# Kernel optimization log

Measured on AMD Instinct MI355X. Metric: run time of the kernel, lower is better.

Reference implementation:

```python
import jax, jax.numpy as jnp
import numpy as np

# Fixed directional 3x3 stencils (order j=0..3 as in the torch module)
_K0 = [[0, 0, 0], [-0.5, 1, -0.5], [0, 0, 0]]
_K1 = [[0, 0, -0.5], [0, 1, 0], [-0.5, 0, 0]]
_K2 = [[0, -0.5, 0], [0, 1, 0], [0, -0.5, 0]]
_K3 = [[-0.5, 0, 0], [0, 1, 0], [0, 0, -0.5]]
KERNELS = jnp.asarray(np.stack([_K0, _K1, _K2, _K3])[:, None], dtype=jnp.float32)  # [4,1,3,3] OIHW
_EPS = 1e-5


def setup_inputs() -> dict:
    key = jax.random.key(0)
    x = jax.random.normal(key, (32, 3, 512, 512), dtype=jnp.float32)
    return {"x": x}


def reference(x):
    # grayscale: [B,1,H,W]
    gray = (0.3 * x[:, 0] + 0.59 * x[:, 1] + 0.11 * x[:, 2])[:, None]
    # one conv with 4 output channels instead of 4 separate 1-channel convs
    ltpe = jax.lax.conv_general_dilated(
        gray, KERNELS, window_strides=(1, 1), padding=((1, 1), (1, 1)),
        dimension_numbers=("NCHW", "OIHW", "NCHW"))  # [B,4,H,W]
    coeffs = (2.0 ** jnp.arange(4, dtype=jnp.float32)) / 15.0  # 2^j / 15
    # sum_j ((ltpe_j + 1) * 0.5) * coeff_j  -> [B,1,H,W]
    out = jnp.einsum("bjhw,j->bhw", (ltpe + 1.0) * 0.5, coeffs)[:, None]
    # InstanceNorm2d(1): per-(batch, channel) normalization over H,W, biased var, no affine
    mean = jnp.mean(out, axis=(2, 3), keepdims=True)
    var = jnp.var(out, axis=(2, 3), keepdims=True)
    out = (out - mean) * jax.lax.rsqrt(var + _EPS)
    return jnp.concatenate([out, out, out], axis=1)  # [B,3,H,W]
```

## Files before the change

kernel.cpp:

```cpp
#include <hip/hip_runtime.h>
#include <hip/hip_fp16.h>

#define IMGS 32
#define H 512
#define W 512
#define NPIX (H * W)
#define NTHR 256
#define RB 8
#define NBANDS (H / RB)
#define C4W (W / 4)

__device__ __forceinline__ float sten(float C, float L, float R, float U, float D,
                                      float UL, float UR, float DL, float DR) {
    const float c0 = 1.0f / 15.0f, c1 = 2.0f / 15.0f;
    const float c2 = 4.0f / 15.0f, c3 = 8.0f / 15.0f;
    const float acc = c0 * (L + R) + c1 * (UR + DL) + c2 * (U + D) + c3 * (UL + DR);
    return fmaf(-0.25f, acc, fmaf(0.5f, C, 0.5f));
}

template <typename ST>
__global__ __launch_bounds__(NTHR, 6) void k1_stencil(
    const float* __restrict__ x, ST* sout, size_t sstride,
    float2* __restrict__ partials)
{
    __shared__ float G[RB + 2][W];

    const int tid  = threadIdx.x;
    const int blk  = blockIdx.x;
    const int img  = blk >> 6;
    const int band = blk & (NBANDS - 1);
    const int r0   = band * RB;

    const float* xbase = x + (size_t)img * 3 * NPIX;
    ST* sbase = sout + (size_t)img * sstride;

#pragma unroll
    for (int it = 0; it < (RB + 2) * C4W / NTHR; ++it) {
        const int idx = it * NTHR + tid;
        const int ri  = idx >> 7;
        const int c4  = idx & (C4W - 1);
        const int gr  = r0 - 1 + ri;
        float4 g4 = make_float4(0.f, 0.f, 0.f, 0.f);
        if ((unsigned)gr < (unsigned)H) {
            const float* p = xbase + gr * W + c4 * 4;
            const float4 r = *(const float4*)p;
            const float4 g = *(const float4*)(p + NPIX);
            const float4 b = *(const float4*)(p + 2 * NPIX);
            g4.x = fmaf(0.3f, r.x, fmaf(0.59f, g.x, 0.11f * b.x));
            g4.y = fmaf(0.3f, r.y, fmaf(0.59f, g.y, 0.11f * b.y));
            g4.z = fmaf(0.3f, r.z, fmaf(0.59f, g.z, 0.11f * b.z));
            g4.w = fmaf(0.3f, r.w, fmaf(0.59f, g.w, 0.11f * b.w));
        }
        *(float4*)&G[ri][c4 * 4] = g4;
    }
    __syncthreads();

    const int c4   = tid & (C4W - 1);
    const int half = tid >> 7;
    const int lr0  = half * (RB / 2);

    float sum = 0.0f, sq = 0.0f;

    float4 a4 = *(const float4*)&G[lr0][c4 * 4];
    float4 b4 = *(const float4*)&G[lr0 + 1][c4 * 4];
    float aL = (c4 == 0) ? 0.0f : G[lr0][c4 * 4 - 1];
    float aR = (c4 == C4W - 1) ? 0.0f : G[lr0][c4 * 4 + 4];
    float bL = (c4 == 0) ? 0.0f : G[lr0 + 1][c4 * 4 - 1];
    float bR = (c4 == C4W - 1) ? 0.0f : G[lr0 + 1][c4 * 4 + 4];

#pragma unroll
    for (int k = 0; k < RB / 2; ++k) {
        const int lr = lr0 + k + 2;
        const float4 d4 = *(const float4*)&G[lr][c4 * 4];
        const float dL = (c4 == 0) ? 0.0f : G[lr][c4 * 4 - 1];
        const float dR = (c4 == C4W - 1) ? 0.0f : G[lr][c4 * 4 + 4];

        float4 o;
        o.x = sten(b4.x, bL,   b4.y, a4.x, d4.x, aL,   a4.y, dL,   d4.y);
        o.y = sten(b4.y, b4.x, b4.z, a4.y, d4.y, a4.x, a4.z, d4.x, d4.z);
        o.z = sten(b4.z, b4.y, b4.w, a4.z, d4.z, a4.y, a4.w, d4.y, d4.w);
        o.w = sten(b4.w, b4.z, bR,   a4.w, d4.w, a4.z, aR,   d4.z, dR);

        sum += (o.x + o.y) + (o.z + o.w);
        sq = fmaf(o.x, o.x, sq); sq = fmaf(o.y, o.y, sq);
        sq = fmaf(o.z, o.z, sq); sq = fmaf(o.w, o.w, sq);

        const size_t off = (size_t)(r0 + half * (RB / 2) + k) * W + c4 * 4;
        if constexpr (sizeof(ST) == 2) {
            union { __half h[4]; float2 f; } u;
            u.h[0] = __float2half_rn(o.x);
            u.h[1] = __float2half_rn(o.y);
            u.h[2] = __float2half_rn(o.z);
            u.h[3] = __float2half_rn(o.w);
            *(float2*)(sbase + off) = u.f;
        } else {
            *(float4*)(sbase + off) = o;
        }

        a4 = b4; aL = bL; aR = bR;
        b4 = d4; bL = dL; bR = dR;
    }

#pragma unroll
    for (int off = 32; off > 0; off >>= 1) {
        sum += __shfl_down(sum, off);
        sq  += __shfl_down(sq, off);
    }
    __syncthreads();
    const int wave = tid >> 6;
    const int lane = tid & 63;
    if (lane == 0) { G[0][wave] = sum; G[0][4 + wave] = sq; }
    __syncthreads();
    if (tid == 0) {
        partials[blk] = make_float2((G[0][0] + G[0][1]) + (G[0][2] + G[0][3]),
                                    (G[0][4] + G[0][5]) + (G[0][6] + G[0][7]));
    }
}

template <typename ST>
__global__ __launch_bounds__(NTHR) void k2_norm(
    const float2* __restrict__ partials, const ST* sin, size_t sstride,
    float* __restrict__ out)
{
    __shared__ float sm[2];

    const int tid = threadIdx.x;
    const int blk = blockIdx.x;
    const int img = blk >> 8;
    const int bi  = blk & 255;

    if (tid < 64) {
        const float2 p = partials[img * NBANDS + tid];
        float S1 = p.x, S2 = p.y;
#pragma unroll
        for (int off = 32; off > 0; off >>= 1) {
            S1 += __shfl_down(S1, off);
            S2 += __shfl_down(S2, off);
        }
        if (tid == 0) {
            const float m = S1 * (1.0f / NPIX);
            const float v = S2 * (1.0f / NPIX) - m * m;
            sm[0] = m;
            sm[1] = rsqrtf(v + 1e-5f);
        }
    }
    __syncthreads();
    const float mean = sm[0];
    const float rstd = sm[1];

    const ST* sb = sin + (size_t)img * sstride;
    float* base = out + (size_t)img * 3 * NPIX;
    const size_t off = (size_t)(bi * NTHR + tid) * 4;

    float4 v;
    if constexpr (sizeof(ST) == 2) {
        union { float2 f; __half h[4]; } u;
        u.f = *(const float2*)(sb + off);
        v.x = __half2float(u.h[0]); v.y = __half2float(u.h[1]);
        v.z = __half2float(u.h[2]); v.w = __half2float(u.h[3]);
    } else {
        v = *(const float4*)(sb + off);
    }
    v.x = (v.x - mean) * rstd;
    v.y = (v.y - mean) * rstd;
    v.z = (v.z - mean) * rstd;
    v.w = (v.w - mean) * rstd;
    *(float4*)(base + off) = v;
    *(float4*)(base + NPIX + off) = v;
    *(float4*)(base + 2 * NPIX + off) = v;
}

extern "C" void kernel_launch(void* const* d_in, const int* in_sizes, int n_in,
                              void* d_out, int out_size, void* d_ws, size_t ws_size,
                              hipStream_t stream) {
    const float* x = (const float*)d_in[0];
    float* out = (float*)d_out;

    const size_t s_bytes = (size_t)IMGS * NPIX * sizeof(__half);
    const size_t need = s_bytes + (size_t)IMGS * NBANDS * sizeof(float2);

    if (ws_size >= need) {
        __half* s = (__half*)d_ws;
        float2* partials = (float2*)((char*)d_ws + s_bytes);
        k1_stencil<__half><<<dim3(IMGS * NBANDS), dim3(NTHR), 0, stream>>>(
            x, s, (size_t)NPIX, partials);
        k2_norm<__half><<<dim3(IMGS * 256), dim3(NTHR), 0, stream>>>(
            partials, s, (size_t)NPIX, out);
    } else {
        float2* partials = (float2*)d_ws;
        k1_stencil<float><<<dim3(IMGS * NBANDS), dim3(NTHR), 0, stream>>>(
            x, out, (size_t)(3 * NPIX), partials);
        k2_norm<float><<<dim3(IMGS * 256), dim3(NTHR), 0, stream>>>(
            partials, out, (size_t)(3 * NPIX), out);
    }
}
```

Measured before the change: 45.75 us.

## Use taller stencil bands, wider norm vectors with nontemporal stores, drop fp32 fallback

```diff
diff --git a/kernel.cpp b/kernel.cpp
--- a/kernel.cpp
+++ b/kernel.cpp
@@ -6,9 +6,14 @@
 #define W 512
 #define NPIX (H * W)
 #define NTHR 256
-#define RB 8
+#define RB 16
 #define NBANDS (H / RB)
 #define C4W (W / 4)
+#define NBLK1 (IMGS * NBANDS)
+#define NBLK2 4096
+#define PXB2 (NTHR * 8)
+
+typedef float vfloat4 __attribute__((ext_vector_type(4)));
 
 __device__ __forceinline__ float sten(float C, float L, float R, float U, float D,
                                       float UL, float UR, float DL, float DR) {
@@ -18,21 +23,21 @@
     return fmaf(-0.25f, acc, fmaf(0.5f, C, 0.5f));
 }
 
-template <typename ST>
-__global__ __launch_bounds__(NTHR, 6) void k1_stencil(
-    const float* __restrict__ x, ST* sout, size_t sstride,
+__global__ __launch_bounds__(NTHR) void k1_stencil(
+    const float* __restrict__ x, __half* __restrict__ sout,
     float2* __restrict__ partials)
 {
     __shared__ float G[RB + 2][W];
+    __shared__ float red[8];
 
     const int tid  = threadIdx.x;
     const int blk  = blockIdx.x;
-    const int img  = blk >> 6;
+    const int img  = blk >> 5;
     const int band = blk & (NBANDS - 1);
     const int r0   = band * RB;
 
     const float* xbase = x + (size_t)img * 3 * NPIX;
-    ST* sbase = sout + (size_t)img * sstride;
+    __half* sbase = sout + (size_t)img * NPIX;
 
 #pragma unroll
     for (int it = 0; it < (RB + 2) * C4W / NTHR; ++it) {
@@ -85,17 +90,12 @@
         sq = fmaf(o.x, o.x, sq); sq = fmaf(o.y, o.y, sq);
         sq = fmaf(o.z, o.z, sq); sq = fmaf(o.w, o.w, sq);
 
-        const size_t off = (size_t)(r0 + half * (RB / 2) + k) * W + c4 * 4;
-        if constexpr (sizeof(ST) == 2) {
-            union { __half h[4]; float2 f; } u;
-            u.h[0] = __float2half_rn(o.x);
-            u.h[1] = __float2half_rn(o.y);
-            u.h[2] = __float2half_rn(o.z);
-            u.h[3] = __float2half_rn(o.w);
-            *(float2*)(sbase + off) = u.f;
-        } else {
-            *(float4*)(sbase + off) = o;
-        }
+        union { __half h[4]; float2 f; } u;
+        u.h[0] = __float2half_rn(o.x);
+        u.h[1] = __float2half_rn(o.y);
+        u.h[2] = __float2half_rn(o.z);
+        u.h[3] = __float2half_rn(o.w);
+        *(float2*)(sbase + (size_t)(r0 + half * (RB / 2) + k) * W + c4 * 4) = u.f;
 
         a4 = b4; aL = bL; aR = bR;
         b4 = d4; bL = dL; bR = dR;
@@ -106,32 +106,33 @@
         sum += __shfl_down(sum, off);
         sq  += __shfl_down(sq, off);
     }
-    __syncthreads();
     const int wave = tid >> 6;
     const int lane = tid & 63;
-    if (lane == 0) { G[0][wave] = sum; G[0][4 + wave] = sq; }
+    if (lane == 0) { red[wave] = sum; red[4 + wave] = sq; }
     __syncthreads();
     if (tid == 0) {
-        partials[blk] = make_float2((G[0][0] + G[0][1]) + (G[0][2] + G[0][3]),
-                                    (G[0][4] + G[0][5]) + (G[0][6] + G[0][7]));
+        partials[blk] = make_float2((red[0] + red[1]) + (red[2] + red[3]),
+                                    (red[4] + red[5]) + (red[6] + red[7]));
     }
 }
 
-template <typename ST>
 __global__ __launch_bounds__(NTHR) void k2_norm(
-    const float2* __restrict__ partials, const ST* sin, size_t sstride,
+    const float2* __restrict__ partials, const __half* __restrict__ sin,
     float* __restrict__ out)
 {
     __shared__ float sm[2];
 
     const int tid = threadIdx.x;
     const int blk = blockIdx.x;
-    const int img = blk >> 8;
-    const int bi  = blk & 255;
+    const int img = blk >> 7;
+    const int bi  = blk & 127;
 
     if (tid < 64) {
-        const float2 p = partials[img * NBANDS + tid];
-        float S1 = p.x, S2 = p.y;
+        float S1 = 0.0f, S2 = 0.0f;
+        if (tid < NBANDS) {
+            const float2 p = partials[img * NBANDS + tid];
+            S1 = p.x; S2 = p.y;
+        }
 #pragma unroll
         for (int off = 32; off > 0; off >>= 1) {
             S1 += __shfl_down(S1, off);
@@ -148,26 +149,29 @@
     const float mean = sm[0];
     const float rstd = sm[1];
 
-    const ST* sb = sin + (size_t)img * sstride;
+    const __half* sb = sin + (size_t)img * NPIX;
     float* base = out + (size_t)img * 3 * NPIX;
-    const size_t off = (size_t)(bi * NTHR + tid) * 4;
+    const size_t off = (size_t)(bi * NTHR + tid) * 8;
 
-    float4 v;
-    if constexpr (sizeof(ST) == 2) {
-        union { float2 f; __half h[4]; } u;
-        u.f = *(const float2*)(sb + off);
-        v.x = __half2float(u.h[0]); v.y = __half2float(u.h[1]);
-        v.z = __half2float(u.h[2]); v.w = __half2float(u.h[3]);
-    } else {
-        v = *(const float4*)(sb + off);
+    union { float4 f4; __half h[8]; } u;
+    u.f4 = *(const float4*)(sb + off);
+
+    vfloat4 v0, v1;
+    v0.x = (__half2float(u.h[0]) - mean) * rstd;
+    v0.y = (__half2float(u.h[1]) - mean) * rstd;
+    v0.z = (__half2float(u.h[2]) - mean) * rstd;
+    v0.w = (__half2float(u.h[3]) - mean) * rstd;
+    v1.x = (__half2float(u.h[4]) - mean) * rstd;
+    v1.y = (__half2float(u.h[5]) - mean) * rstd;
+    v1.z = (__half2float(u.h[6]) - mean) * rstd;
+    v1.w = (__half2float(u.h[7]) - mean) * rstd;
+
+#pragma unroll
+    for (int ch = 0; ch < 3; ++ch) {
+        float* p = base + (size_t)ch * NPIX + off;
+        __builtin_nontemporal_store(v0, (vfloat4*)p);
+        __builtin_nontemporal_store(v1, (vfloat4*)(p + 4));
     }
-    v.x = (v.x - mean) * rstd;
-    v.y = (v.y - mean) * rstd;
-    v.z = (v.z - mean) * rstd;
-    v.w = (v.w - mean) * rstd;
-    *(float4*)(base + off) = v;
-    *(float4*)(base + NPIX + off) = v;
-    *(float4*)(base + 2 * NPIX + off) = v;
 }
 
 extern "C" void kernel_launch(void* const* d_in, const int* in_sizes, int n_in,
@@ -176,21 +180,9 @@
     const float* x = (const float*)d_in[0];
     float* out = (float*)d_out;
 
-    const size_t s_bytes = (size_t)IMGS * NPIX * sizeof(__half);
-    const size_t need = s_bytes + (size_t)IMGS * NBANDS * sizeof(float2);
+    __half* s = (__half*)d_ws;
+    float2* partials = (float2*)((char*)d_ws + (size_t)IMGS * NPIX * sizeof(__half));
 
-    if (ws_size >= need) {
-        __half* s = (__half*)d_ws;
-        float2* partials = (float2*)((char*)d_ws + s_bytes);
-        k1_stencil<__half><<<dim3(IMGS * NBANDS), dim3(NTHR), 0, stream>>>(
-            x, s, (size_t)NPIX, partials);
-        k2_norm<__half><<<dim3(IMGS * 256), dim3(NTHR), 0, stream>>>(
-            partials, s, (size_t)NPIX, out);
-    } else {
-        float2* partials = (float2*)d_ws;
-        k1_stencil<float><<<dim3(IMGS * NBANDS), dim3(NTHR), 0, stream>>>(
-            x, out, (size_t)(3 * NPIX), partials);
-        k2_norm<float><<<dim3(IMGS * 256), dim3(NTHR), 0, stream>>>(
-            partials, out, (size_t)(3 * NPIX), out);
-    }
+    k1_stencil<<<dim3(NBLK1), dim3(NTHR), 0, stream>>>(x, s, partials);
+    k2_norm<<<dim3(NBLK2), dim3(NTHR), 0, stream>>>(partials, s, out);
 }
```

Result: slower. 63.77 us (+39.4%).
